# Kernel tuning notes

Measured on AMD Instinct MI355X. Metric: run time of the kernel, lower is better.

Reference implementation:

```python
import jax, jax.numpy as jnp
import numpy as np

NH = 8
QCH = 256
KCH = 256
VCH = 256


def setup_inputs() -> dict:
    key = jax.random.key(0)
    ks = jax.random.split(key, 6)
    B, C, H, W = 8, 512, 28, 28
    return {
        "inputs": jax.random.normal(ks[0], (B, C, H, W), jnp.float32),
        "inputs_st": jax.random.normal(ks[1], (B, C, H, W), jnp.float32),
        "Wq": jax.random.normal(ks[2], (QCH, C), jnp.float32) * 0.02,
        "bq": jnp.zeros((QCH,), jnp.float32),
        "Wkv": jax.random.normal(ks[3], (KCH + VCH, C), jnp.float32) * 0.02,
        "bkv": jnp.zeros((KCH + VCH,), jnp.float32),
        "Wo": jax.random.normal(ks[4], (512, VCH), jnp.float32) * 0.02,
        "bo": jnp.zeros((512,), jnp.float32),
    }


def reference(inputs, inputs_st, Wq, bq, Wkv, bkv, Wo, bo):
    B, C, H, W = inputs.shape
    dkh = KCH // NH  # scale uses k-channels per head, as in source

    # 1x1 conv projections == channel matmuls
    q = jnp.einsum('bchw,oc->bohw', inputs, Wq) + bq[None, :, None, None]
    kv = jnp.einsum('bchw,oc->bohw', inputs_st, Wkv) + bkv[None, :, None, None]
    k, v = kv[:, :KCH], kv[:, KCH:]

    # split heads: (B, Nh, ch//Nh, H, W)
    q = q.reshape(B, NH, QCH // NH, H, W) * (dkh ** -0.5)
    k = k.reshape(B, NH, KCH // NH, H, W)
    v = v.reshape(B, NH, VCH // NH, H, W)

    flat_q = q.reshape(B, NH, QCH // NH, H * W)
    flat_k = k.reshape(B, NH, KCH // NH, H * W)
    flat_v = v.reshape(B, NH, VCH // NH, H * W)

    # logits: (B, Nh, HqWq, HW) = q^T k
    logits = jnp.einsum('bnds,bndt->bnst', flat_q, flat_k)
    # NOTE: source applies softmax over dim=1 (the head axis), not the key axis
    weights = jax.nn.softmax(logits, axis=1)
    # attn_out: (B, Nh, HqWq, dvh)
    attn_out = jnp.einsum('bnst,bndt->bnsd', weights, flat_v)
    # faithful raw reshapes (no transpose), matching torch.reshape semantics
    attn_out = attn_out.reshape(B, NH, VCH // NH, H, W)
    attn_out = attn_out.reshape(B, VCH, H, W)

    out = jnp.einsum('bchw,oc->bohw', attn_out, Wo) + bo[None, :, None, None]
    return out
```

## Files before the change

kernel.cpp:

```cpp
#include <hip/hip_runtime.h>

#define SS 784
#define NQE 1605632

typedef float f32x4 __attribute__((ext_vector_type(4)));
typedef short s16x8 __attribute__((ext_vector_type(8)));

__device__ inline ushort f2bf(float f) {
    union { float f; unsigned u; } v; v.f = f;
    return (ushort)((v.u + 0x7fff + ((v.u >> 16) & 1)) >> 16);
}
__device__ inline float bf2f(ushort h) {
    union { unsigned u; float f; } v; v.u = ((unsigned)h) << 16;
    return v.f;
}
__device__ inline unsigned cvt_pk_bf16(float lo, float hi) {
    unsigned r;
    asm("v_cvt_pk_bf16_f32 %0, %1, %2" : "=v"(r) : "v"(lo), "v"(hi));
    return r;
}

__global__ __launch_bounds__(256) void transpose_cvt2(const float* __restrict__ X0,
                                                      const float* __restrict__ X1,
                                                      ushort* __restrict__ Xt0,
                                                      ushort* __restrict__ Xt1) {
    __shared__ ushort Ts[64][72];
    const int tid = threadIdx.x;
    const int p0 = blockIdx.x * 64, c0 = blockIdx.y * 64;
    const int z  = blockIdx.z;
    const int b  = z & 7;
    const float*  X  = (z < 8) ? X0 : X1;
    ushort*       Xt = (z < 8) ? Xt0 : Xt1;
    const int cr = tid >> 2, ch = (tid & 3) * 16;
    if (p0 + ch < SS) {
        const float* src = X + ((size_t)b * 512 + c0 + cr) * SS + p0 + ch;
        #pragma unroll
        for (int jj = 0; jj < 4; ++jj) {
            float4 v = *(const float4*)(src + jj * 4);
            Ts[ch + jj * 4 + 0][cr] = f2bf(v.x);
            Ts[ch + jj * 4 + 1][cr] = f2bf(v.y);
            Ts[ch + jj * 4 + 2][cr] = f2bf(v.z);
            Ts[ch + jj * 4 + 3][cr] = f2bf(v.w);
        }
    } else {
        #pragma unroll
        for (int j = 0; j < 16; ++j) Ts[ch + j][cr] = 0;
    }
    __syncthreads();
    const int pr = tid >> 2, cc = (tid & 3) * 16;
    if (p0 + pr < SS) {
        ushort* dst = Xt + ((size_t)b * SS + p0 + pr) * 512 + c0 + cc;
        *(s16x8*)dst       = *(const s16x8*)&Ts[pr][cc];
        *(s16x8*)(dst + 8) = *(const s16x8*)&Ts[pr][cc + 8];
    }
}

__global__ __launch_bounds__(256) void gemm_qkv(const ushort* __restrict__ xt_q,
                                                const ushort* __restrict__ xt_kv,
                                                const float* __restrict__ Wq,
                                                const float* __restrict__ bq,
                                                const float* __restrict__ Wkv,
                                                const float* __restrict__ bkv,
                                                ushort* __restrict__ qt,
                                                ushort* __restrict__ kt,
                                                ushort* __restrict__ vv,
                                                float qscale) {
    __shared__ ushort As[128 * 40];
    __shared__ ushort Bs[128 * 40];
    const int id  = blockIdx.x;
    const int b   = id & 7;
    const int sub = id >> 3;
    const int oy  = sub % 6;
    const int p0  = (sub / 6) * 128;
    const int mode = (oy < 2) ? 0 : (oy < 4 ? 1 : 2);
    const ushort* Xt  = (mode == 0) ? xt_q : xt_kv;
    const float* Wg   = (mode == 0) ? Wq : Wkv;
    const float* bias = (mode == 0) ? bq : bkv;
    const int o0w = (mode == 0) ? oy * 128 : (oy - 2) * 128;

    const int tid = threadIdx.x;
    const int lane = tid & 63, wave = tid >> 6;
    const int wm = wave >> 1, wn = wave & 1;
    const int lg = lane >> 4, lm = lane & 15;
    const int srow = tid >> 1, shalf = (tid & 1) * 16;

    const f32x4 Z4 = {0.f, 0.f, 0.f, 0.f};
    const s16x8 Z8 = {0, 0, 0, 0, 0, 0, 0, 0};
    f32x4 acc[4][4];
    #pragma unroll
    for (int m = 0; m < 4; ++m)
        #pragma unroll
        for (int n = 0; n < 4; ++n) acc[m][n] = Z4;

    for (int c0 = 0; c0 < 512; c0 += 32) {
        __syncthreads();
        {
            const float* src = Wg + (size_t)(o0w + srow) * 512 + c0 + shalf;
            ushort tmp[16];
            #pragma unroll
            for (int jj = 0; jj < 4; ++jj) {
                float4 v = *(const float4*)(src + jj * 4);
                tmp[jj * 4 + 0] = f2bf(v.x); tmp[jj * 4 + 1] = f2bf(v.y);
                tmp[jj * 4 + 2] = f2bf(v.z); tmp[jj * 4 + 3] = f2bf(v.w);
            }
            *(s16x8*)&As[srow * 40 + shalf]     = *(s16x8*)&tmp[0];
            *(s16x8*)&As[srow * 40 + shalf + 8] = *(s16x8*)&tmp[8];
        }
        {
            int p = p0 + srow;
            s16x8 v0 = Z8, v1 = Z8;
            if (p < SS) {
                const ushort* src = Xt + ((size_t)b * SS + p) * 512 + c0 + shalf;
                v0 = *(const s16x8*)src;
                v1 = *(const s16x8*)(src + 8);
            }
            *(s16x8*)&Bs[srow * 40 + shalf]     = v0;
            *(s16x8*)&Bs[srow * 40 + shalf + 8] = v1;
        }
        __syncthreads();
        s16x8 af[4], bf[4];
        #pragma unroll
        for (int m = 0; m < 4; ++m) af[m] = *(const s16x8*)&As[(wm * 64 + m * 16 + lm) * 40 + 8 * lg];
        #pragma unroll
        for (int n = 0; n < 4; ++n) bf[n] = *(const s16x8*)&Bs[(wn * 64 + n * 16 + lm) * 40 + 8 * lg];
        #pragma unroll
        for (int m = 0; m < 4; ++m)
            #pragma unroll
            for (int n = 0; n < 4; ++n)
                acc[m][n] = __builtin_amdgcn_mfma_f32_16x16x32_bf16(af[m], bf[n], acc[m][n], 0, 0, 0);
    }

    if (mode < 2) {
        ushort* outT = (mode == 0) ? qt : kt;
        const float scale = (mode == 0) ? qscale : 1.0f;
        #pragma unroll
        for (int m = 0; m < 4; ++m) {
            const int o = o0w + wm * 64 + m * 16 + 4 * lg;
            float bv[4];
            #pragma unroll
            for (int r = 0; r < 4; ++r) bv[r] = bias[o + r];
            #pragma unroll
            for (int n = 0; n < 4; ++n) {
                const int p = p0 + wn * 64 + n * 16 + lm;
                if (p < SS) {
                    ushort4 w;
                    w.x = f2bf((acc[m][n][0] + bv[0]) * scale);
                    w.y = f2bf((acc[m][n][1] + bv[1]) * scale);
                    w.z = f2bf((acc[m][n][2] + bv[2]) * scale);
                    w.w = f2bf((acc[m][n][3] + bv[3]) * scale);
                    *(ushort4*)&outT[((size_t)b * SS + p) * 256 + o] = w;
                }
            }
        }
    } else {
        #pragma unroll
        for (int m = 0; m < 4; ++m) {
            const int ob = o0w + wm * 64 + m * 16 + 4 * lg;
            float bv[4];
            #pragma unroll
            for (int r = 0; r < 4; ++r) bv[r] = bias[ob + r];
            #pragma unroll
            for (int n = 0; n < 4; ++n) {
                const int p = p0 + wn * 64 + n * 16 + lm;
                if (p < SS) {
                    #pragma unroll
                    for (int r = 0; r < 4; ++r) {
                        const int c = ob - 256 + r;
                        vv[((size_t)b * 256 + c) * SS + p] = f2bf(acc[m][n][r] + bv[r]);
                    }
                }
            }
        }
    }
}

__global__ __launch_bounds__(256) void gemm_out(const ushort* __restrict__ A,
                                                const float* __restrict__ Wg,
                                                const float* __restrict__ bias,
                                                float* __restrict__ outp) {
    __shared__ ushort As[128 * 40];
    __shared__ ushort Bs[128 * 40];
    const int tid = threadIdx.x;
    const int lane = tid & 63, wave = tid >> 6;
    const int wm = wave >> 1, wn = wave & 1;
    const int lg = lane >> 4, lm = lane & 15;
    const int b  = blockIdx.x;
    const int p0 = blockIdx.y * 128;
    const int o0 = blockIdx.z * 128;
    const int srow = tid >> 1, shalf = (tid & 1) * 16;

    const f32x4 Z4 = {0.f, 0.f, 0.f, 0.f};
    const s16x8 Z8 = {0, 0, 0, 0, 0, 0, 0, 0};
    f32x4 acc[4][4];
    #pragma unroll
    for (int m = 0; m < 4; ++m)
        #pragma unroll
        for (int n = 0; n < 4; ++n) acc[m][n] = Z4;

    for (int c0 = 0; c0 < 256; c0 += 32) {
        __syncthreads();
        {
            int p = p0 + srow;
            s16x8 v0 = Z8, v1 = Z8;
            if (p < SS) {
                const ushort* src = A + ((size_t)b * SS + p) * 256 + c0 + shalf;
                v0 = *(const s16x8*)src;
                v1 = *(const s16x8*)(src + 8);
            }
            *(s16x8*)&As[srow * 40 + shalf]     = v0;
            *(s16x8*)&As[srow * 40 + shalf + 8] = v1;
        }
        {
            const float* src = Wg + (size_t)(o0 + srow) * 256 + c0 + shalf;
            ushort tmp[16];
            #pragma unroll
            for (int jj = 0; jj < 4; ++jj) {
                float4 v = *(const float4*)(src + jj * 4);
                tmp[jj * 4 + 0] = f2bf(v.x); tmp[jj * 4 + 1] = f2bf(v.y);
                tmp[jj * 4 + 2] = f2bf(v.z); tmp[jj * 4 + 3] = f2bf(v.w);
            }
            *(s16x8*)&Bs[srow * 40 + shalf]     = *(s16x8*)&tmp[0];
            *(s16x8*)&Bs[srow * 40 + shalf + 8] = *(s16x8*)&tmp[8];
        }
        __syncthreads();
        s16x8 af[4], bf[4];
        #pragma unroll
        for (int m = 0; m < 4; ++m) af[m] = *(const s16x8*)&As[(wm * 64 + m * 16 + lm) * 40 + 8 * lg];
        #pragma unroll
        for (int n = 0; n < 4; ++n) bf[n] = *(const s16x8*)&Bs[(wn * 64 + n * 16 + lm) * 40 + 8 * lg];
        #pragma unroll
        for (int m = 0; m < 4; ++m)
            #pragma unroll
            for (int n = 0; n < 4; ++n)
                acc[m][n] = __builtin_amdgcn_mfma_f32_16x16x32_bf16(af[m], bf[n], acc[m][n], 0, 0, 0);
    }

    #pragma unroll
    for (int n = 0; n < 4; ++n) {
        const int o = o0 + wn * 64 + n * 16 + lm;
        const float bv = bias[o];
        #pragma unroll
        for (int m = 0; m < 4; ++m) {
            const int p = p0 + wm * 64 + m * 16 + 4 * lg;
            if (p < SS) {
                f32x4 v;
                #pragma unroll
                for (int r = 0; r < 4; ++r) v[r] = acc[m][n][r] + bv;
                *(f32x4*)&outp[((size_t)b * 512 + o) * SS + p] = v;
            }
        }
    }
}

#define KROW 280
#define VROW 40
#define PROW 40

__global__ __launch_bounds__(256, 3) void attn_mfma(const ushort* __restrict__ qt,
                                                    const ushort* __restrict__ kt,
                                                    const ushort* __restrict__ vv,
                                                    ushort* __restrict__ pb,
                                                    ushort* __restrict__ p4) {
    __shared__ ushort ks[32 * KROW];
    __shared__ ushort vs[256 * VROW];
    __shared__ ushort pls[4 * 2 * 16 * PROW];
    const int tid  = threadIdx.x;
    const int lane = tid & 63;
    const int wave = tid >> 6;
    const int b     = blockIdx.x;
    const int stile = blockIdx.y / 5;
    const int ts    = blockIdx.y % 5;
    int strip = stile * 4 + wave;
    const bool valid = (strip < 49);
    if (!valid) strip = 48;
    const int s0 = strip * 16;

    const int lg = lane >> 4, lm = lane & 15;
    const s16x8 Z8 = {0, 0, 0, 0, 0, 0, 0, 0};
    const f32x4 Z4 = {0.f, 0.f, 0.f, 0.f};

    s16x8 qf[8];
    const ushort* qbase = qt + ((size_t)b * SS + s0 + lm) * 256 + 8 * lg;
    #pragma unroll
    for (int n = 0; n < 8; ++n) qf[n] = *(const s16x8*)(qbase + n * 32);

    f32x4 oacc[8][2];
    #pragma unroll
    for (int n = 0; n < 8; ++n) { oacc[n][0] = Z4; oacc[n][1] = Z4; }

    const ushort* ktb = kt + (size_t)b * SS * 256;
    const ushort* vb  = vv + (size_t)b * 256 * SS;
    ushort* pbase = pls + wave * (2 * 16 * PROW);

    for (int ti = ts * 5; ti < ts * 5 + 5; ++ti) {
        const int t0 = ti * 32;
        __syncthreads();
        {
            const int row = tid >> 3, ce = (tid & 7) * 32;
            const int t = t0 + row;
            const ushort* src = ktb + (size_t)t * 256 + ce;
            #pragma unroll
            for (int j = 0; j < 4; ++j) {
                s16x8 v = (t < SS) ? *(const s16x8*)(src + 8 * j) : Z8;
                *(s16x8*)&ks[row * KROW + ce + 8 * j] = v;
            }
        }
        {
            const ushort* src = vb + (size_t)tid * SS + t0;
            #pragma unroll
            for (int j = 0; j < 4; ++j) {
                s16x8 v = (t0 + 8 * j < SS) ? *(const s16x8*)(src + 8 * j) : Z8;
                *(s16x8*)&vs[tid * VROW + 8 * j] = v;
            }
        }
        __syncthreads();

        unsigned pku[2][8][2];
        #pragma unroll
        for (int h = 0; h < 2; ++h) {
            f32x4 lacc[8];
            #pragma unroll
            for (int n = 0; n < 8; ++n) {
                s16x8 ak = *(const s16x8*)&ks[(h * 16 + lm) * KROW + n * 32 + 8 * lg];
                lacc[n] = __builtin_amdgcn_mfma_f32_16x16x32_bf16(ak, qf[n], Z4, 0, 0, 0);
            }
            #pragma unroll
            for (int r = 0; r < 4; ++r) {
                float e[8]; float sum = 0.f;
                #pragma unroll
                for (int n = 0; n < 8; ++n) { e[n] = exp2f(lacc[n][r]); sum += e[n]; }
                float inv;
                asm("v_rcp_f32 %0, %1" : "=v"(inv) : "v"(sum));
                #pragma unroll
                for (int n = 0; n < 8; ++n) lacc[n][r] = e[n] * inv;
            }
            #pragma unroll
            for (int n = 0; n < 8; ++n) {
                pku[h][n][0] = cvt_pk_bf16(lacc[n][0], lacc[n][1]);
                pku[h][n][1] = cvt_pk_bf16(lacc[n][2], lacc[n][3]);
            }
        }

        #pragma unroll
        for (int n = 0; n < 8; ++n) {
            ushort* pw = pbase + (n & 1) * (16 * PROW);
            uint2 w0; w0.x = pku[0][n][0]; w0.y = pku[0][n][1];
            *(uint2*)&pw[lm * PROW + 4 * lg] = w0;
            uint2 w1; w1.x = pku[1][n][0]; w1.y = pku[1][n][1];
            *(uint2*)&pw[lm * PROW + 16 + 4 * lg] = w1;
            s16x8 pbf = *(const s16x8*)&pw[lm * PROW + 8 * lg];
            #pragma unroll
            for (int dh = 0; dh < 2; ++dh) {
                s16x8 va = *(const s16x8*)&vs[(n * 32 + dh * 16 + lm) * VROW + 8 * lg];
                oacc[n][dh] = __builtin_amdgcn_mfma_f32_16x16x32_bf16(va, pbf, oacc[n][dh], 0, 0, 0);
            }
        }
    }

    if (valid) {
        ushort* part = (ts < 4) ? (pb + (size_t)ts * NQE) : p4;
        const size_t base = (size_t)b * 200704 + (size_t)s0 * 32 + lm * 32 + 4 * lg;
        #pragma unroll
        for (int n = 0; n < 8; ++n) {
            #pragma unroll
            for (int dh = 0; dh < 2; ++dh) {
                uint2 w;
                w.x = cvt_pk_bf16(oacc[n][dh][0], oacc[n][dh][1]);
                w.y = cvt_pk_bf16(oacc[n][dh][2], oacc[n][dh][3]);
                *(uint2*)&part[base + n * 25088 + dh * 16] = w;
            }
        }
    }
}

__global__ __launch_bounds__(256) void sum5t(const ushort* __restrict__ a0,
                                             const ushort* __restrict__ a1,
                                             const ushort* __restrict__ a2,
                                             const ushort* __restrict__ a3,
                                             const ushort* __restrict__ a4,
                                             ushort* __restrict__ outb) {
    __shared__ ushort Ts[64][72];
    const int tid = threadIdx.x;
    const int p0 = blockIdx.x * 64, c0 = blockIdx.y * 64, b = blockIdx.z;
    const int cr = tid >> 2, ch = (tid & 3) * 16;
    if (p0 + ch < SS) {
        const size_t off = ((size_t)b * 256 + c0 + cr) * SS + p0 + ch;
        #pragma unroll
        for (int jj = 0; jj < 2; ++jj) {
            s16x8 v0 = *(const s16x8*)(a0 + off + 8 * jj);
            s16x8 v1 = *(const s16x8*)(a1 + off + 8 * jj);
            s16x8 v2 = *(const s16x8*)(a2 + off + 8 * jj);
            s16x8 v3 = *(const s16x8*)(a3 + off + 8 * jj);
            s16x8 v4 = *(const s16x8*)(a4 + off + 8 * jj);
            #pragma unroll
            for (int j = 0; j < 8; ++j) {
                float s = bf2f((ushort)v0[j]) + bf2f((ushort)v1[j]) + bf2f((ushort)v2[j])
                        + bf2f((ushort)v3[j]) + bf2f((ushort)v4[j]);
                Ts[ch + jj * 8 + j][cr] = f2bf(s);
            }
        }
    } else {
        #pragma unroll
        for (int j = 0; j < 16; ++j) Ts[ch + j][cr] = 0;
    }
    __syncthreads();
    const int pr = tid >> 2, cc = (tid & 3) * 16;
    if (p0 + pr < SS) {
        ushort* dst = outb + ((size_t)b * SS + p0 + pr) * 256 + c0 + cc;
        *(s16x8*)dst       = *(const s16x8*)&Ts[pr][cc];
        *(s16x8*)(dst + 8) = *(const s16x8*)&Ts[pr][cc + 8];
    }
}

extern "C" void kernel_launch(void* const* d_in, const int* in_sizes, int n_in,
                              void* d_out, int out_size, void* d_ws, size_t ws_size,
                              hipStream_t stream) {
    const float* inputs    = (const float*)d_in[0];
    const float* inputs_st = (const float*)d_in[1];
    const float* Wq        = (const float*)d_in[2];
    const float* bq        = (const float*)d_in[3];
    const float* Wkv       = (const float*)d_in[4];
    const float* bkv       = (const float*)d_in[5];
    const float* Wo        = (const float*)d_in[6];
    const float* bo        = (const float*)d_in[7];
    float* out = (float*)d_out;

    ushort* W     = (ushort*)d_ws;
    ushort* xt_q  = W;
    ushort* xt_kv = W + 2 * (size_t)NQE;
    ushort* qt    = W + 4 * (size_t)NQE;
    ushort* kt    = W + 5 * (size_t)NQE;
    ushort* vv    = W + 6 * (size_t)NQE;
    ushort* p4    = W + 7 * (size_t)NQE;
    ushort* sumb  = qt;

    const float qscale = (float)(1.4426950408889634 / 5.656854249492380195);

    transpose_cvt2<<<dim3(13, 8, 16), dim3(256), 0, stream>>>(inputs, inputs_st, xt_q, xt_kv);
    gemm_qkv<<<dim3(336), dim3(256), 0, stream>>>(xt_q, xt_kv, Wq, bq, Wkv, bkv, qt, kt, vv, qscale);
    attn_mfma<<<dim3(8, 65), dim3(256), 0, stream>>>(qt, kt, vv, W, p4);
    sum5t<<<dim3(13, 4, 8), dim3(256), 0, stream>>>(W, W + (size_t)NQE, W + 2 * (size_t)NQE,
                                                    W + 3 * (size_t)NQE, p4, sumb);
    gemm_out<<<dim3(8, 7, 4), dim3(256), 0, stream>>>(sumb, Wo, bo, out);
}
```

Baseline: 91.85 us.

## Prefetch K/V tiles into registers, shrink LDS padding, reorder sum5t grid

The attention kernel now loads the next K/V tile from global memory into registers while the current tile is being computed. The registers are written to LDS after the next barrier, so global load latency overlaps with the MFMA and softmax work. The LDS row padding drops from 280/40/40 to 260/36/36, which changes bank-conflict behaviour and lowers LDS use. The sum5t grid is permuted so batch is the fastest-varying block index. The prefetch adds register pressure under launch_bounds(256,3), which could cause spills.

```diff
diff --git a/kernel.cpp b/kernel.cpp
--- a/kernel.cpp
+++ b/kernel.cpp
@@ -252,9 +252,9 @@
     }
 }
 
-#define KROW 280
-#define VROW 40
-#define PROW 40
+#define KROW 260
+#define VROW 36
+#define PROW 36
 
 __global__ __launch_bounds__(256, 3) void attn_mfma(const ushort* __restrict__ qt,
                                                     const ushort* __restrict__ kt,
@@ -292,28 +292,33 @@
     const ushort* vb  = vv + (size_t)b * 256 * SS;
     ushort* pbase = pls + wave * (2 * 16 * PROW);
 
-    for (int ti = ts * 5; ti < ts * 5 + 5; ++ti) {
-        const int t0 = ti * 32;
-        __syncthreads();
-        {
-            const int row = tid >> 3, ce = (tid & 7) * 32;
-            const int t = t0 + row;
-            const ushort* src = ktb + (size_t)t * 256 + ce;
-            #pragma unroll
-            for (int j = 0; j < 4; ++j) {
-                s16x8 v = (t < SS) ? *(const s16x8*)(src + 8 * j) : Z8;
-                *(s16x8*)&ks[row * KROW + ce + 8 * j] = v;
-            }
-        }
-        {
-            const ushort* src = vb + (size_t)tid * SS + t0;
-            #pragma unroll
-            for (int j = 0; j < 4; ++j) {
-                s16x8 v = (t0 + 8 * j < SS) ? *(const s16x8*)(src + 8 * j) : Z8;
-                *(s16x8*)&vs[tid * VROW + 8 * j] = v;
-            }
-        }
-        __syncthreads();
+    const int krow = tid >> 3, kce = (tid & 7) * 32;
+
+    s16x8 kreg[4], vreg[4];
+    auto LOADKV = [&](int t0) {
+        const ushort* ksrc = ktb + (size_t)(t0 + krow) * 256 + kce;
+        const bool kok = (t0 + krow) < SS;
+        #pragma unroll
+        for (int j = 0; j < 4; ++j)
+            kreg[j] = kok ? *(const s16x8*)(ksrc + 8 * j) : Z8;
+        const ushort* vsrc = vb + (size_t)tid * SS + t0;
+        #pragma unroll
+        for (int j = 0; j < 4; ++j)
+            vreg[j] = (t0 + 8 * j < SS) ? *(const s16x8*)(vsrc + 8 * j) : Z8;
+    };
+
+    LOADKV(ts * 160);
+    for (int ti = 0; ti < 5; ++ti) {
+        const int t0 = ts * 160 + ti * 32;
+        __syncthreads();
+        #pragma unroll
+        for (int j = 0; j < 4; ++j)
+            *(s16x8*)&ks[krow * KROW + kce + 8 * j] = kreg[j];
+        #pragma unroll
+        for (int j = 0; j < 4; ++j)
+            *(s16x8*)&vs[tid * VROW + 8 * j] = vreg[j];
+        __syncthreads();
+        if (ti < 4) LOADKV(t0 + 32);
 
         unsigned pku[2][8][2];
         #pragma unroll
@@ -381,7 +386,7 @@
                                              ushort* __restrict__ outb) {
     __shared__ ushort Ts[64][72];
     const int tid = threadIdx.x;
-    const int p0 = blockIdx.x * 64, c0 = blockIdx.y * 64, b = blockIdx.z;
+    const int b = blockIdx.x, p0 = blockIdx.y * 64, c0 = blockIdx.z * 64;
     const int cr = tid >> 2, ch = (tid & 3) * 16;
     if (p0 + ch < SS) {
         const size_t off = ((size_t)b * 256 + c0 + cr) * SS + p0 + ch;
@@ -439,7 +444,7 @@
     transpose_cvt2<<<dim3(13, 8, 16), dim3(256), 0, stream>>>(inputs, inputs_st, xt_q, xt_kv);
     gemm_qkv<<<dim3(336), dim3(256), 0, stream>>>(xt_q, xt_kv, Wq, bq, Wkv, bkv, qt, kt, vv, qscale);
     attn_mfma<<<dim3(8, 65), dim3(256), 0, stream>>>(qt, kt, vv, W, p4);
-    sum5t<<<dim3(13, 4, 8), dim3(256), 0, stream>>>(W, W + (size_t)NQE, W + 2 * (size_t)NQE,
+    sum5t<<<dim3(8, 13, 4), dim3(256), 0, stream>>>(W, W + (size_t)NQE, W + 2 * (size_t)NQE,
                                                     W + 3 * (size_t)NQE, p4, sumb);
     gemm_out<<<dim3(8, 7, 4), dim3(256), 0, stream>>>(sumb, Wo, bo, out);
 }
```

Measured after the change: 118.6 us. 29.1% more time.

## Double-buffer attention K/V tiles via direct global-to-LDS loads with XOR swizzle

Applied to the files above, without the earlier changes.

The attention kernel now stages K and V tiles straight into LDS with global_load_lds, double-buffered so the next tile's loads overlap the current tile's MFMA work. Padded LDS rows are replaced by an XOR swizzle to avoid bank conflicts. The tail tile past the sequence end is zeroed explicitly after loading. Occupancy hint drops from 3 to 2 blocks per CU because LDS use grows, and the sum5t grid order is permuted so batch is the fastest-varying index.

```diff
diff --git a/kernel.cpp b/kernel.cpp
--- a/kernel.cpp
+++ b/kernel.cpp
@@ -18,6 +18,11 @@
     unsigned r;
     asm("v_cvt_pk_bf16_f32 %0, %1, %2" : "=v"(r) : "v"(lo), "v"(hi));
     return r;
+}
+__device__ inline void gl_lds16(const ushort* g, ushort* l) {
+    __builtin_amdgcn_global_load_lds(
+        (const __attribute__((address_space(1))) void*)g,
+        (__attribute__((address_space(3))) void*)l, 16, 0, 0);
 }
 
 __global__ __launch_bounds__(256) void transpose_cvt2(const float* __restrict__ X0,
@@ -252,18 +257,16 @@
     }
 }
 
-#define KROW 280
-#define VROW 40
-#define PROW 40
-
-__global__ __launch_bounds__(256, 3) void attn_mfma(const ushort* __restrict__ qt,
+#define PROW 36
+
+__global__ __launch_bounds__(256, 2) void attn_mfma(const ushort* __restrict__ qt,
                                                     const ushort* __restrict__ kt,
                                                     const ushort* __restrict__ vv,
                                                     ushort* __restrict__ pb,
                                                     ushort* __restrict__ p4) {
-    __shared__ ushort ks[32 * KROW];
-    __shared__ ushort vs[256 * VROW];
-    __shared__ ushort pls[4 * 2 * 16 * PROW];
+    __shared__ ushort ks[2][32 * 256];
+    __shared__ ushort vs[2][256 * 32];
+    __shared__ ushort pls[4][16 * PROW];
     const int tid  = threadIdx.x;
     const int lane = tid & 63;
     const int wave = tid >> 6;
@@ -276,7 +279,6 @@
     const int s0 = strip * 16;
 
     const int lg = lane >> 4, lm = lane & 15;
-    const s16x8 Z8 = {0, 0, 0, 0, 0, 0, 0, 0};
     const f32x4 Z4 = {0.f, 0.f, 0.f, 0.f};
 
     s16x8 qf[8];
@@ -290,30 +292,46 @@
 
     const ushort* ktb = kt + (size_t)b * SS * 256;
     const ushort* vb  = vv + (size_t)b * 256 * SS;
-    ushort* pbase = pls + wave * (2 * 16 * PROW);
-
-    for (int ti = ts * 5; ti < ts * 5 + 5; ++ti) {
-        const int t0 = ti * 32;
-        __syncthreads();
-        {
-            const int row = tid >> 3, ce = (tid & 7) * 32;
-            const int t = t0 + row;
-            const ushort* src = ktb + (size_t)t * 256 + ce;
-            #pragma unroll
-            for (int j = 0; j < 4; ++j) {
-                s16x8 v = (t < SS) ? *(const s16x8*)(src + 8 * j) : Z8;
-                *(s16x8*)&ks[row * KROW + ce + 8 * j] = v;
-            }
-        }
-        {
-            const ushort* src = vb + (size_t)tid * SS + t0;
-            #pragma unroll
-            for (int j = 0; j < 4; ++j) {
-                s16x8 v = (t0 + 8 * j < SS) ? *(const s16x8*)(src + 8 * j) : Z8;
-                *(s16x8*)&vs[tid * VROW + 8 * j] = v;
-            }
-        }
-        __syncthreads();
+    ushort* pw = pls[wave];
+
+    auto STAGE = [&](int buf, int t0) {
+        #pragma unroll
+        for (int it = 0; it < 4; ++it) {
+            const int ci = it * 256 + tid;
+            const int kr = ci >> 5, kcb = ci & 31;
+            gl_lds16(ktb + (size_t)(t0 + kr) * 256 + ((kcb ^ (kr & 7)) << 3), &ks[buf][ci << 3]);
+        }
+        #pragma unroll
+        for (int it = 0; it < 4; ++it) {
+            const int ci = it * 256 + tid;
+            const int vc = ci >> 2, vtb = ci & 3;
+            gl_lds16(vb + (size_t)vc * SS + t0 + ((vtb ^ (vc & 3)) << 3), &vs[buf][ci << 3]);
+        }
+    };
+
+    STAGE(0, ts * 160);
+    int cur = 0;
+    for (int ti = 0; ti < 5; ++ti) {
+        if (ti < 4) {
+            STAGE(cur ^ 1, ts * 160 + ti * 32 + 32);
+            asm volatile("s_waitcnt vmcnt(8)" ::: "memory");
+        } else {
+            asm volatile("s_waitcnt vmcnt(0)" ::: "memory");
+        }
+        __builtin_amdgcn_s_barrier();
+        __builtin_amdgcn_sched_barrier(0);
+
+        if (ts == 4 && ti == 4) {
+            {   const int row = 16 + (tid >> 4), col = (tid & 15) * 16;
+                uint4 z = {0, 0, 0, 0};
+                *(uint4*)&ks[cur][row * 256 + col]     = z;
+                *(uint4*)&ks[cur][row * 256 + col + 8] = z;
+                const int c = tid;
+                *(uint4*)&vs[cur][c * 32 + ((2 ^ (c & 3)) << 3)] = z;
+                *(uint4*)&vs[cur][c * 32 + ((3 ^ (c & 3)) << 3)] = z;
+            }
+            __syncthreads();
+        }
 
         unsigned pku[2][8][2];
         #pragma unroll
@@ -321,7 +339,7 @@
             f32x4 lacc[8];
             #pragma unroll
             for (int n = 0; n < 8; ++n) {
-                s16x8 ak = *(const s16x8*)&ks[(h * 16 + lm) * KROW + n * 32 + 8 * lg];
+                s16x8 ak = *(const s16x8*)&ks[cur][(h * 16 + lm) * 256 + (((4 * n + lg) ^ (lm & 7)) << 3)];
                 lacc[n] = __builtin_amdgcn_mfma_f32_16x16x32_bf16(ak, qf[n], Z4, 0, 0, 0);
             }
             #pragma unroll
@@ -343,7 +361,6 @@
 
         #pragma unroll
         for (int n = 0; n < 8; ++n) {
-            ushort* pw = pbase + (n & 1) * (16 * PROW);
             uint2 w0; w0.x = pku[0][n][0]; w0.y = pku[0][n][1];
             *(uint2*)&pw[lm * PROW + 4 * lg] = w0;
             uint2 w1; w1.x = pku[1][n][0]; w1.y = pku[1][n][1];
@@ -351,10 +368,12 @@
             s16x8 pbf = *(const s16x8*)&pw[lm * PROW + 8 * lg];
             #pragma unroll
             for (int dh = 0; dh < 2; ++dh) {
-                s16x8 va = *(const s16x8*)&vs[(n * 32 + dh * 16 + lm) * VROW + 8 * lg];
+                s16x8 va = *(const s16x8*)&vs[cur][(n * 32 + dh * 16 + lm) * 32 + ((lg ^ (lm & 3)) << 3)];
                 oacc[n][dh] = __builtin_amdgcn_mfma_f32_16x16x32_bf16(va, pbf, oacc[n][dh], 0, 0, 0);
             }
         }
+        __builtin_amdgcn_s_barrier();
+        cur ^= 1;
     }
 
     if (valid) {
@@ -381,7 +400,7 @@
                                              ushort* __restrict__ outb) {
     __shared__ ushort Ts[64][72];
     const int tid = threadIdx.x;
-    const int p0 = blockIdx.x * 64, c0 = blockIdx.y * 64, b = blockIdx.z;
+    const int b = blockIdx.x, p0 = blockIdx.y * 64, c0 = blockIdx.z * 64;
     const int cr = tid >> 2, ch = (tid & 3) * 16;
     if (p0 + ch < SS) {
         const size_t off = ((size_t)b * 256 + c0 + cr) * SS + p0 + ch;
@@ -439,7 +458,7 @@
     transpose_cvt2<<<dim3(13, 8, 16), dim3(256), 0, stream>>>(inputs, inputs_st, xt_q, xt_kv);
     gemm_qkv<<<dim3(336), dim3(256), 0, stream>>>(xt_q, xt_kv, Wq, bq, Wkv, bkv, qt, kt, vv, qscale);
     attn_mfma<<<dim3(8, 65), dim3(256), 0, stream>>>(qt, kt, vv, W, p4);
-    sum5t<<<dim3(13, 4, 8), dim3(256), 0, stream>>>(W, W + (size_t)NQE, W + 2 * (size_t)NQE,
+    sum5t<<<dim3(8, 13, 4), dim3(256), 0, stream>>>(W, W + (size_t)NQE, W + 2 * (size_t)NQE,
                                                     W + 3 * (size_t)NQE, p4, sumb);
     gemm_out<<<dim3(8, 7, 4), dim3(256), 0, stream>>>(sumb, Wo, bo, out);
 }
```

Measured after the change: 97.11 us. 5.7% more time.
